# Optimization experiments

Hardware: AMD Instinct MI355X
Metric: run time of the kernel (lower is better)

Reference implementation:

```python
import jax, jax.numpy as jnp
import numpy as np

EMB = 1024
HEADS = 16
HEAD_DIM = EMB // HEADS
B, S = 4, 2048


def setup_inputs() -> dict:
    key = jax.random.key(0)
    ks = jax.random.split(key, 9)
    sc = 1.0 / np.sqrt(EMB)
    x = jax.random.normal(ks[0], (B, S, EMB), dtype=jnp.float32)
    Wq = jax.random.normal(ks[1], (EMB, EMB), dtype=jnp.float32) * sc
    bq = jax.random.normal(ks[2], (EMB,), dtype=jnp.float32) * 0.02
    Wk = jax.random.normal(ks[3], (EMB, EMB), dtype=jnp.float32) * sc
    bk = jax.random.normal(ks[4], (EMB,), dtype=jnp.float32) * 0.02
    Wv = jax.random.normal(ks[5], (EMB, EMB), dtype=jnp.float32) * sc
    bv = jax.random.normal(ks[6], (EMB,), dtype=jnp.float32) * 0.02
    Wo = jax.random.normal(ks[7], (EMB, EMB), dtype=jnp.float32) * sc
    bo = jax.random.normal(ks[8], (EMB,), dtype=jnp.float32) * 0.02
    # causal mask: 1 where allowed (lower triangular), 0 elsewhere
    causal_mask = jnp.tril(jnp.ones((S, S), dtype=jnp.int32))[None, None]
    return {"x": x, "Wq": Wq, "bq": bq, "Wk": Wk, "bk": bk,
            "Wv": Wv, "bv": bv, "Wo": Wo, "bo": bo,
            "causal_mask": causal_mask}


def reference(x, Wq, bq, Wk, bk, Wv, bv, Wo, bo, causal_mask):
    bs, seq, _ = x.shape
    # nn.Linear: x @ W.T + b; then view [bs, seq, H, hd] and transpose to [bs, H, seq, hd]
    def proj(W, b):
        return (x @ W.T + b).reshape(bs, seq, HEADS, HEAD_DIM).transpose(0, 2, 1, 3)
    q, k, v = proj(Wq, bq), proj(Wk, bk), proj(Wv, bv)
    scale = 1.0 / np.sqrt(HEAD_DIM).astype(np.float32)
    dots = jnp.einsum('bhqd,bhkd->bhqk', q, k) * scale  # [B, H, S, S]
    dots = jnp.where(causal_mask == 0, -jnp.inf, dots)
    attn = jax.nn.softmax(dots, axis=-1)
    out = jnp.einsum('bhqk,bhkd->bhqd', attn, v)  # [B, H, S, hd]
    out = out.transpose(0, 2, 1, 3).reshape(bs, seq, EMB)
    return out @ Wo.T + bo
```

## Files before the change

kernel.cpp:

```cpp
#include <hip/hip_runtime.h>
#include <hip/hip_bf16.h>

typedef __attribute__((ext_vector_type(8))) short short8;
typedef __attribute__((ext_vector_type(4))) float floatx4;

#define B_    4
#define S_    2048
#define EMB_  1024
#define NH_   16
#define HD_   64

#if __has_builtin(__builtin_amdgcn_exp2f)
#define EXP2F(x) __builtin_amdgcn_exp2f(x)
#else
#define EXP2F(x) exp2f(x)
#endif

__device__ __forceinline__ void async_cp16(const void* g, void* l) {
  __builtin_amdgcn_global_load_lds(
      (const __attribute__((address_space(1))) unsigned int*)g,
      (__attribute__((address_space(3))) unsigned int*)l, 16, 0, 0);
}

__device__ __forceinline__ ushort4 cvt4(const float4 f) {
  __bf16 t[4] = {(__bf16)f.x, (__bf16)f.y, (__bf16)f.z, (__bf16)f.w};
  return *(const ushort4*)t;
}

__device__ __forceinline__ short8 pack8(const float4 a, const float4 b) {
  union { short8 s; ushort4 u[2]; } r;
  r.u[0] = cvt4(a);
  r.u[1] = cvt4(b);
  return r.s;
}

__global__ __launch_bounds__(256)
void cvt_kernel(const float* __restrict__ x,
                const float* __restrict__ wq, const float* __restrict__ wk,
                const float* __restrict__ wv, const float* __restrict__ wo,
                const float* __restrict__ bq, const float* __restrict__ bk,
                const float* __restrict__ bv,
                __bf16* __restrict__ xb, __bf16* __restrict__ Wcat,
                __bf16* __restrict__ Wob, float* __restrict__ bcat)
{
  const int NX4 = 2097152;
  const int NW4 = 262144;
  int g = blockIdx.x * 256 + threadIdx.x;
  if (g < NX4) {
    *(ushort4*)(xb + (size_t)g * 4) = cvt4(*(const float4*)(x + (size_t)g * 4));
    return;
  }
  g -= NX4;
  if (g < 3 * NW4) {
    const float* src = (g < NW4) ? wq : (g < 2 * NW4) ? wk : wv;
    const int gg = (g < NW4) ? g : (g < 2 * NW4) ? g - NW4 : g - 2 * NW4;
    *(ushort4*)(Wcat + (size_t)g * 4) = cvt4(*(const float4*)(src + (size_t)gg * 4));
    return;
  }
  g -= 3 * NW4;
  if (g < NW4) {
    *(ushort4*)(Wob + (size_t)g * 4) = cvt4(*(const float4*)(wo + (size_t)g * 4));
    return;
  }
  g -= NW4;
  if (g < 768) {
    const float* src = (g < 256) ? bq : (g < 512) ? bk : bv;
    *(float4*)(bcat + (size_t)g * 4) = *(const float4*)(src + (size_t)(g & 255) * 4);
  }
}

__global__ __launch_bounds__(256)
void gemm_qkv_kernel(const __bf16* __restrict__ A, const __bf16* __restrict__ W,
                     const float* __restrict__ bcat,
                     __bf16* __restrict__ Qb, __bf16* __restrict__ Kb,
                     __bf16* __restrict__ Vb)
{
  __shared__ __attribute__((aligned(16))) __bf16 As[128 * 32];
  __shared__ __attribute__((aligned(16))) __bf16 Ws[128 * 32];
  const int tid  = threadIdx.x;
  const int wave = tid >> 6, lane = tid & 63;
  const int l15  = lane & 15, quad = lane >> 4;
  const int wm   = wave >> 1, wn = wave & 1;
  const int bm   = blockIdx.y * 128;
  const int bn   = blockIdx.x * 128;
  const int widx = bn >> 10;
  const float QS = 0.180336880f;

  floatx4 acc[4][4];
#pragma unroll
  for (int i = 0; i < 4; ++i)
#pragma unroll
    for (int j = 0; j < 4; ++j) acc[i][j] = (floatx4){0.f, 0.f, 0.f, 0.f};

  const int srow = tid >> 2;
  const int gcol = (((tid & 3) ^ ((tid >> 3) & 3)) << 3);
  const int xsw  = (l15 >> 1) & 3;
  const __bf16* Ag = A + (size_t)(bm + srow) * 1024 + gcol;
  const __bf16* Wg = W + (size_t)(bn + srow) * 1024 + gcol;
  __bf16* AsD = As + tid * 8;
  __bf16* WsD = Ws + tid * 8;

  for (int k0 = 0; k0 < 1024; k0 += 32) {
    __syncthreads();
    async_cp16(Ag + k0,             AsD);
    async_cp16(Ag + k0 + 64 * 1024, AsD + 2048);
    async_cp16(Wg + k0,             WsD);
    async_cp16(Wg + k0 + 64 * 1024, WsD + 2048);
    __syncthreads();
    short8 af[4], wf[4];
#pragma unroll
    for (int mi = 0; mi < 4; ++mi)
      af[mi] = *(const short8*)(As + ((wm * 64 + mi * 16 + l15) << 5) + ((quad ^ xsw) << 3));
#pragma unroll
    for (int ni = 0; ni < 4; ++ni)
      wf[ni] = *(const short8*)(Ws + ((wn * 64 + ni * 16 + l15) << 5) + ((quad ^ xsw) << 3));
#pragma unroll
    for (int mi = 0; mi < 4; ++mi)
#pragma unroll
      for (int ni = 0; ni < 4; ++ni)
        acc[mi][ni] = __builtin_amdgcn_mfma_f32_16x16x32_bf16(af[mi], wf[ni], acc[mi][ni], 0, 0, 0);
  }

#pragma unroll
  for (int ni = 0; ni < 4; ++ni) {
    const int n  = bn + wn * 64 + ni * 16 + l15;
    const float bvb = bcat[n];
    const int np = n & 1023;
    const int h = np >> 6, d = np & 63;
#pragma unroll
    for (int mi = 0; mi < 4; ++mi) {
      const int m0 = bm + wm * 64 + mi * 16 + quad * 4;
      const int b = m0 >> 11, s0 = m0 & 2047;
      floatx4 v = acc[mi][ni];
      if (widx == 0) {
        const size_t base = (size_t)(b * 16 + h) * (S_ * 64) + d;
#pragma unroll
        for (int r = 0; r < 4; ++r)
          Qb[base + (size_t)(s0 + r) * 64] = (__bf16)((v[r] + bvb) * QS);
      } else if (widx == 1) {
        const size_t base = (size_t)(b * 16 + h) * (S_ * 64) + d;
#pragma unroll
        for (int r = 0; r < 4; ++r)
          Kb[base + (size_t)(s0 + r) * 64] = (__bf16)(v[r] + bvb);
      } else {
        const size_t base = ((size_t)(b * 16 + h) * 64 + d) * S_ + s0;
        union { ushort4 u4; unsigned short u[4]; } pk;
#pragma unroll
        for (int r = 0; r < 4; ++r) {
          __bf16 hv = (__bf16)(v[r] + bvb);
          pk.u[r] = *(unsigned short*)&hv;
        }
        *(ushort4*)(Vb + base) = pk.u4;
      }
    }
  }
}

__device__ __forceinline__ void softmax_update_pf(
    floatx4* s, float& mrun, float& lsum, floatx4* oacc,
    short8& pf0, short8& pf1)
{
  float t0 = fmaxf(fmaxf(s[0][0], s[0][1]), fmaxf(s[0][2], s[0][3]));
  float t1 = fmaxf(fmaxf(s[1][0], s[1][1]), fmaxf(s[1][2], s[1][3]));
  float t2 = fmaxf(fmaxf(s[2][0], s[2][1]), fmaxf(s[2][2], s[2][3]));
  float t3 = fmaxf(fmaxf(s[3][0], s[3][1]), fmaxf(s[3][2], s[3][3]));
  float tmax = fmaxf(fmaxf(t0, t1), fmaxf(t2, t3));
  tmax = fmaxf(tmax, __shfl_xor(tmax, 16));
  tmax = fmaxf(tmax, __shfl_xor(tmax, 32));

  const float mold = mrun;
  if (!__all(tmax <= mold + 8.0f)) {
    const float mnew = fmaxf(mold, tmax);
    const float alpha = EXP2F(mold - mnew);
#pragma unroll
    for (int ni = 0; ni < 4; ++ni)
#pragma unroll
      for (int r = 0; r < 4; ++r) oacc[ni][r] *= alpha;
    lsum *= alpha;
    mrun = mnew;
  }
  const float m = mrun;

  float4 p0, p1, p2, p3;
  p0.x = EXP2F(s[0][0] - m); p0.y = EXP2F(s[0][1] - m);
  p0.z = EXP2F(s[0][2] - m); p0.w = EXP2F(s[0][3] - m);
  p1.x = EXP2F(s[1][0] - m); p1.y = EXP2F(s[1][1] - m);
  p1.z = EXP2F(s[1][2] - m); p1.w = EXP2F(s[1][3] - m);
  p2.x = EXP2F(s[2][0] - m); p2.y = EXP2F(s[2][1] - m);
  p2.z = EXP2F(s[2][2] - m); p2.w = EXP2F(s[2][3] - m);
  p3.x = EXP2F(s[3][0] - m); p3.y = EXP2F(s[3][1] - m);
  p3.z = EXP2F(s[3][2] - m); p3.w = EXP2F(s[3][3] - m);

  lsum += ((p0.x + p0.y) + (p0.z + p0.w)) + ((p1.x + p1.y) + (p1.z + p1.w))
        + ((p2.x + p2.y) + (p2.z + p2.w)) + ((p3.x + p3.y) + (p3.z + p3.w));

  pf0 = pack8(p0, p2);
  pf1 = pack8(p1, p3);
}

__global__ __launch_bounds__(256, 2)
void attn_kernel(__bf16* __restrict__ Q, const __bf16* __restrict__ K,
                 const __bf16* __restrict__ Vt)
{
  __shared__ __attribute__((aligned(16))) __bf16 Ks[64 * 72];
  __shared__ __attribute__((aligned(16))) __bf16 Vs[64 * 72];

  const int tid  = threadIdx.x;
  const int wave = tid >> 6, lane = tid & 63;
  const int l15  = lane & 15, quad = lane >> 4;
  const int qtA  = blockIdx.x, bh = blockIdx.y;
  const size_t hb = (size_t)bh * (S_ * 64);
  const float MASKV = -1.0e30f;

  const int srow = tid >> 3;
  const int scol = (tid & 7) << 3;
  const int prow = ((srow >> 2) & 1) * 32 + ((srow >> 3) & 3) * 4 + (srow & 3);

  for (int qsel = 0; qsel < 2; ++qsel) {
    const int qt = qsel ? (15 - qtA) : qtA;
    const int qw = qt * 128 + wave * 32;
    const int myqA = qw + l15;
    const int myqB = qw + 16 + l15;
    const int nsub = 2 * qt + 2;

    const __bf16* qpA = Q + hb + (size_t)myqA * 64 + quad * 8;
    const __bf16* qpB = Q + hb + (size_t)myqB * 64 + quad * 8;
    short8 aqA0 = *(const short8*)(qpA);
    short8 aqA1 = *(const short8*)(qpA + 32);
    short8 aqB0 = *(const short8*)(qpB);
    short8 aqB1 = *(const short8*)(qpB + 32);

    floatx4 oaccA[4], oaccB[4];
#pragma unroll
    for (int j = 0; j < 4; ++j) {
      oaccA[j] = (floatx4){0.f, 0.f, 0.f, 0.f};
      oaccB[j] = (floatx4){0.f, 0.f, 0.f, 0.f};
    }
    float lsumA = 0.f, lsumB = 0.f;
    float mrunA = MASKV, mrunB = MASKV;

    uint4 kreg0, kreg1, vreg0, vreg1;
    {
      const __bf16* kp = K  + hb + (size_t)srow * 64 + scol;
      const __bf16* vp = Vt + hb + (size_t)srow * S_ + scol;
      kreg0 = *(const uint4*)kp;
      kreg1 = *(const uint4*)(kp + 32 * 64);
      vreg0 = *(const uint4*)vp;
      vreg1 = *(const uint4*)(vp + (size_t)32 * S_);
    }

    for (int kt = 0; kt < nsub; ++kt) {
      __syncthreads();
      *(uint4*)(&Ks[prow * 72 + scol])        = kreg0;
      *(uint4*)(&Ks[(prow + 16) * 72 + scol]) = kreg1;
      *(uint4*)(&Vs[srow * 72 + scol])        = vreg0;
      *(uint4*)(&Vs[(srow + 32) * 72 + scol]) = vreg1;
      __syncthreads();

      if (kt + 1 < nsub) {
        const __bf16* kp = K  + hb + (size_t)((kt + 1) * 64 + srow) * 64 + scol;
        const __bf16* vp = Vt + hb + (size_t)srow * S_ + (kt + 1) * 64 + scol;
        kreg0 = *(const uint4*)kp;
        kreg1 = *(const uint4*)(kp + 32 * 64);
        vreg0 = *(const uint4*)vp;
        vreg1 = *(const uint4*)(vp + (size_t)32 * S_);
      }

      if (kt * 64 <= qw + 31) {
        floatx4 sA[4], sB[4];
#pragma unroll
        for (int j = 0; j < 4; ++j) {
          sA[j] = (floatx4){0.f, 0.f, 0.f, 0.f};
          sB[j] = (floatx4){0.f, 0.f, 0.f, 0.f};
        }
#pragma unroll
        for (int kk = 0; kk < 2; ++kk) {
          const short8 aqa = kk ? aqA1 : aqA0;
          const short8 aqb = kk ? aqB1 : aqB0;
          short8 bk[4];
#pragma unroll
          for (int ni = 0; ni < 4; ++ni)
            bk[ni] = *(const short8*)(&Ks[(ni * 16 + l15) * 72 + kk * 32 + quad * 8]);
#pragma unroll
          for (int ni = 0; ni < 4; ++ni)
            sA[ni] = __builtin_amdgcn_mfma_f32_16x16x32_bf16(bk[ni], aqa, sA[ni], 0, 0, 0);
#pragma unroll
          for (int ni = 0; ni < 4; ++ni)
            sB[ni] = __builtin_amdgcn_mfma_f32_16x16x32_bf16(bk[ni], aqb, sB[ni], 0, 0, 0);
        }

        const int kb2 = kt * 64 + quad * 8;
        if (kt * 64 + 63 > qw) {
#pragma unroll
          for (int ni = 0; ni < 4; ++ni)
#pragma unroll
            for (int r = 0; r < 4; ++r) {
              const int kvg = kb2 + ((ni & 1) << 5) + ((ni >> 1) << 2) + r;
              if (kvg > myqA) sA[ni][r] = MASKV;
            }
        }
        if (kt * 64 + 63 > qw + 16) {
#pragma unroll
          for (int ni = 0; ni < 4; ++ni)
#pragma unroll
            for (int r = 0; r < 4; ++r) {
              const int kvg = kb2 + ((ni & 1) << 5) + ((ni >> 1) << 2) + r;
              if (kvg > myqB) sB[ni][r] = MASKV;
            }
        }

        short8 pfA0, pfA1, pfB0, pfB1;
        softmax_update_pf(sA, mrunA, lsumA, oaccA, pfA0, pfA1);
        softmax_update_pf(sB, mrunB, lsumB, oaccB, pfB0, pfB1);

#pragma unroll
        for (int kk = 0; kk < 2; ++kk) {
          short8 bv[4];
#pragma unroll
          for (int ni = 0; ni < 4; ++ni)
            bv[ni] = *(const short8*)(&Vs[(ni * 16 + l15) * 72 + kk * 32 + quad * 8]);
          const short8 pfA = kk ? pfA1 : pfA0;
          const short8 pfB = kk ? pfB1 : pfB0;
#pragma unroll
          for (int ni = 0; ni < 4; ++ni)
            oaccA[ni] = __builtin_amdgcn_mfma_f32_16x16x32_bf16(bv[ni], pfA, oaccA[ni], 0, 0, 0);
#pragma unroll
          for (int ni = 0; ni < 4; ++ni)
            oaccB[ni] = __builtin_amdgcn_mfma_f32_16x16x32_bf16(bv[ni], pfB, oaccB[ni], 0, 0, 0);
        }
      }
    }

    {
      float l = lsumA;
      l += __shfl_xor(l, 16);
      l += __shfl_xor(l, 32);
      const float inv = 1.0f / fmaxf(l, 1e-20f);
      const size_t rowb = hb + (size_t)myqA * 64;
#pragma unroll
      for (int ni = 0; ni < 4; ++ni) {
        float4 o;
        o.x = oaccA[ni][0] * inv;
        o.y = oaccA[ni][1] * inv;
        o.z = oaccA[ni][2] * inv;
        o.w = oaccA[ni][3] * inv;
        *(ushort4*)(Q + rowb + ni * 16 + quad * 4) = cvt4(o);
      }
    }
    {
      float l = lsumB;
      l += __shfl_xor(l, 16);
      l += __shfl_xor(l, 32);
      const float inv = 1.0f / fmaxf(l, 1e-20f);
      const size_t rowb = hb + (size_t)myqB * 64;
#pragma unroll
      for (int ni = 0; ni < 4; ++ni) {
        float4 o;
        o.x = oaccB[ni][0] * inv;
        o.y = oaccB[ni][1] * inv;
        o.z = oaccB[ni][2] * inv;
        o.w = oaccB[ni][3] * inv;
        *(ushort4*)(Q + rowb + ni * 16 + quad * 4) = cvt4(o);
      }
    }
  }
}

__global__ __launch_bounds__(256)
void gemm_o_kernel(const __bf16* __restrict__ A, const __bf16* __restrict__ W,
                   const float* __restrict__ bias, float* __restrict__ out)
{
  __shared__ __attribute__((aligned(16))) __bf16 As[128 * 32];
  __shared__ __attribute__((aligned(16))) __bf16 Ws[128 * 32];
  const int tid  = threadIdx.x;
  const int wave = tid >> 6, lane = tid & 63;
  const int l15  = lane & 15, quad = lane >> 4;
  const int wm   = wave >> 1, wn = wave & 1;
  const int bm   = blockIdx.y * 128;
  const int bn   = blockIdx.x * 128;

  floatx4 acc[4][4];
#pragma unroll
  for (int i = 0; i < 4; ++i)
#pragma unroll
    for (int j = 0; j < 4; ++j) acc[i][j] = (floatx4){0.f, 0.f, 0.f, 0.f};

  const int srow = tid >> 2;
  const int gcol = (((tid & 3) ^ ((tid >> 3) & 3)) << 3);
  const int xsw  = (l15 >> 1) & 3;
  const __bf16* Wg = W + (size_t)(bn + srow) * 1024 + gcol;
  const int bb = bm >> 11;
  const int ss = (bm & 2047) + srow;
  __bf16* AsD = As + tid * 8;
  __bf16* WsD = Ws + tid * 8;

  for (int k0 = 0; k0 < 1024; k0 += 32) {
    const int c = k0 + gcol, h = c >> 6, dd = c & 63;
    const __bf16* pa0 = A + (((size_t)(bb * 16 + h) * S_) + ss) * 64 + dd;
    __syncthreads();
    async_cp16(pa0,           AsD);
    async_cp16(pa0 + 64 * 64, AsD + 2048);
    async_cp16(Wg + k0,             WsD);
    async_cp16(Wg + k0 + 64 * 1024, WsD + 2048);
    __syncthreads();

    short8 af[4], wf[4];
#pragma unroll
    for (int mi = 0; mi < 4; ++mi)
      af[mi] = *(const short8*)(As + ((wm * 64 + mi * 16 + l15) << 5) + ((quad ^ xsw) << 3));
#pragma unroll
    for (int ni = 0; ni < 4; ++ni)
      wf[ni] = *(const short8*)(Ws + ((wn * 64 + ni * 16 + l15) << 5) + ((quad ^ xsw) << 3));
#pragma unroll
    for (int mi = 0; mi < 4; ++mi)
#pragma unroll
      for (int ni = 0; ni < 4; ++ni)
        acc[mi][ni] = __builtin_amdgcn_mfma_f32_16x16x32_bf16(af[mi], wf[ni], acc[mi][ni], 0, 0, 0);
  }

#pragma unroll
  for (int ni = 0; ni < 4; ++ni) {
    const int n = bn + wn * 64 + ni * 16 + l15;
    const float bvb = bias[n];
#pragma unroll
    for (int mi = 0; mi < 4; ++mi) {
      const int m0 = bm + wm * 64 + mi * 16 + quad * 4;
      floatx4 v = acc[mi][ni];
#pragma unroll
      for (int r = 0; r < 4; ++r)
        out[(size_t)(m0 + r) * 1024 + n] = v[r] + bvb;
    }
  }
}

extern "C" void kernel_launch(void* const* d_in, const int* in_sizes, int n_in,
                              void* d_out, int out_size, void* d_ws, size_t ws_size,
                              hipStream_t stream) {
  const float* x  = (const float*)d_in[0];
  const float* Wq = (const float*)d_in[1];
  const float* bq = (const float*)d_in[2];
  const float* Wk = (const float*)d_in[3];
  const float* bk = (const float*)d_in[4];
  const float* Wv = (const float*)d_in[5];
  const float* bv = (const float*)d_in[6];
  const float* Wo = (const float*)d_in[7];
  const float* bo = (const float*)d_in[8];

  const size_t BUF = (size_t)B_ * NH_ * S_ * HD_;
  __bf16* ws   = (__bf16*)d_ws;
  __bf16* xb   = ws;
  __bf16* Wcat = ws + 8388608;
  __bf16* Wob  = ws + 11534336;
  __bf16* Qb   = ws + 12582912;
  float*  bcat = (float*)(ws + 20971520);
  __bf16* Kb   = (__bf16*)d_out;
  __bf16* Vb   = (__bf16*)d_out + BUF;

  dim3 blk(256);
  cvt_kernel<<<12291, blk, 0, stream>>>(x, Wq, Wk, Wv, Wo, bq, bk, bv,
                                        xb, Wcat, Wob, bcat);
  gemm_qkv_kernel<<<dim3(24, 64), blk, 0, stream>>>(xb, Wcat, bcat, Qb, Kb, Vb);
  attn_kernel<<<dim3(8, 64), blk, 0, stream>>>(Qb, Kb, Vb);
  gemm_o_kernel<<<dim3(8, 64), blk, 0, stream>>>(Qb, Wob, bo, (float*)d_out);
}
```

Measured before the change: 276.3 us.

## Fuse x fp32-to-bf16 conversion into QKV GEMM loads, raise MFMA wave priority

The separate pass that converted x to bf16 in the workspace is removed. The QKV GEMM now loads fp32 x directly into registers, prefetched one k-step ahead, and packs it to bf16 before storing to LDS. This drops a full 32 MB read and 16 MB write and shrinks the conversion launch. The cost is that each x tile is read as fp32 and converted once for each of the 24 N-blocks, replacing the async global-to-LDS copy with register loads. The attention kernel also wraps its MFMA groups in s_setprio to favour matrix-issuing waves.

```diff
diff --git a/kernel.cpp b/kernel.cpp
--- a/kernel.cpp
+++ b/kernel.cpp
@@ -35,22 +35,15 @@
 }
 
 __global__ __launch_bounds__(256)
-void cvt_kernel(const float* __restrict__ x,
-                const float* __restrict__ wq, const float* __restrict__ wk,
+void cvt_kernel(const float* __restrict__ wq, const float* __restrict__ wk,
                 const float* __restrict__ wv, const float* __restrict__ wo,
                 const float* __restrict__ bq, const float* __restrict__ bk,
                 const float* __restrict__ bv,
-                __bf16* __restrict__ xb, __bf16* __restrict__ Wcat,
-                __bf16* __restrict__ Wob, float* __restrict__ bcat)
+                __bf16* __restrict__ Wcat, __bf16* __restrict__ Wob,
+                float* __restrict__ bcat)
 {
-  const int NX4 = 2097152;
   const int NW4 = 262144;
   int g = blockIdx.x * 256 + threadIdx.x;
-  if (g < NX4) {
-    *(ushort4*)(xb + (size_t)g * 4) = cvt4(*(const float4*)(x + (size_t)g * 4));
-    return;
-  }
-  g -= NX4;
   if (g < 3 * NW4) {
     const float* src = (g < NW4) ? wq : (g < 2 * NW4) ? wk : wv;
     const int gg = (g < NW4) ? g : (g < 2 * NW4) ? g - NW4 : g - 2 * NW4;
@@ -70,7 +63,7 @@
 }
 
 __global__ __launch_bounds__(256)
-void gemm_qkv_kernel(const __bf16* __restrict__ A, const __bf16* __restrict__ W,
+void gemm_qkv_kernel(const float* __restrict__ X, const __bf16* __restrict__ W,
                      const float* __restrict__ bcat,
                      __bf16* __restrict__ Qb, __bf16* __restrict__ Kb,
                      __bf16* __restrict__ Vb)
@@ -95,18 +88,30 @@
   const int srow = tid >> 2;
   const int gcol = (((tid & 3) ^ ((tid >> 3) & 3)) << 3);
   const int xsw  = (l15 >> 1) & 3;
-  const __bf16* Ag = A + (size_t)(bm + srow) * 1024 + gcol;
+  const float*  Ag = X + (size_t)(bm + srow) * 1024 + gcol;
   const __bf16* Wg = W + (size_t)(bn + srow) * 1024 + gcol;
   __bf16* AsD = As + tid * 8;
   __bf16* WsD = Ws + tid * 8;
 
+  float4 a00, a01, a10, a11;
+  a00 = *(const float4*)(Ag);
+  a01 = *(const float4*)(Ag + 4);
+  a10 = *(const float4*)(Ag + 64 * 1024);
+  a11 = *(const float4*)(Ag + 64 * 1024 + 4);
+
   for (int k0 = 0; k0 < 1024; k0 += 32) {
     __syncthreads();
-    async_cp16(Ag + k0,             AsD);
-    async_cp16(Ag + k0 + 64 * 1024, AsD + 2048);
+    *(short8*)(AsD)        = pack8(a00, a01);
+    *(short8*)(AsD + 2048) = pack8(a10, a11);
     async_cp16(Wg + k0,             WsD);
     async_cp16(Wg + k0 + 64 * 1024, WsD + 2048);
     __syncthreads();
+    if (k0 + 32 < 1024) {
+      a00 = *(const float4*)(Ag + k0 + 32);
+      a01 = *(const float4*)(Ag + k0 + 36);
+      a10 = *(const float4*)(Ag + k0 + 32 + 64 * 1024);
+      a11 = *(const float4*)(Ag + k0 + 36 + 64 * 1024);
+    }
     short8 af[4], wf[4];
 #pragma unroll
     for (int mi = 0; mi < 4; ++mi)
@@ -281,12 +286,14 @@
 #pragma unroll
           for (int ni = 0; ni < 4; ++ni)
             bk[ni] = *(const short8*)(&Ks[(ni * 16 + l15) * 72 + kk * 32 + quad * 8]);
+          __builtin_amdgcn_s_setprio(1);
 #pragma unroll
           for (int ni = 0; ni < 4; ++ni)
             sA[ni] = __builtin_amdgcn_mfma_f32_16x16x32_bf16(bk[ni], aqa, sA[ni], 0, 0, 0);
 #pragma unroll
           for (int ni = 0; ni < 4; ++ni)
             sB[ni] = __builtin_amdgcn_mfma_f32_16x16x32_bf16(bk[ni], aqb, sB[ni], 0, 0, 0);
+          __builtin_amdgcn_s_setprio(0);
         }
 
         const int kb2 = kt * 64 + quad * 8;
@@ -321,12 +328,14 @@
             bv[ni] = *(const short8*)(&Vs[(ni * 16 + l15) * 72 + kk * 32 + quad * 8]);
           const short8 pfA = kk ? pfA1 : pfA0;
           const short8 pfB = kk ? pfB1 : pfB0;
+          __builtin_amdgcn_s_setprio(1);
 #pragma unroll
           for (int ni = 0; ni < 4; ++ni)
             oaccA[ni] = __builtin_amdgcn_mfma_f32_16x16x32_bf16(bv[ni], pfA, oaccA[ni], 0, 0, 0);
 #pragma unroll
           for (int ni = 0; ni < 4; ++ni)
             oaccB[ni] = __builtin_amdgcn_mfma_f32_16x16x32_bf16(bv[ni], pfB, oaccB[ni], 0, 0, 0);
+          __builtin_amdgcn_s_setprio(0);
         }
       }
     }
@@ -448,18 +457,17 @@
 
   const size_t BUF = (size_t)B_ * NH_ * S_ * HD_;
   __bf16* ws   = (__bf16*)d_ws;
-  __bf16* xb   = ws;
-  __bf16* Wcat = ws + 8388608;
-  __bf16* Wob  = ws + 11534336;
-  __bf16* Qb   = ws + 12582912;
-  float*  bcat = (float*)(ws + 20971520);
+  __bf16* Wcat = ws;
+  __bf16* Wob  = ws + 3145728;
+  __bf16* Qb   = ws + 4194304;
+  float*  bcat = (float*)(ws + 12582912);
   __bf16* Kb   = (__bf16*)d_out;
   __bf16* Vb   = (__bf16*)d_out + BUF;
 
   dim3 blk(256);
-  cvt_kernel<<<12291, blk, 0, stream>>>(x, Wq, Wk, Wv, Wo, bq, bk, bv,
-                                        xb, Wcat, Wob, bcat);
-  gemm_qkv_kernel<<<dim3(24, 64), blk, 0, stream>>>(xb, Wcat, bcat, Qb, Kb, Vb);
+  cvt_kernel<<<4099, blk, 0, stream>>>(Wq, Wk, Wv, Wo, bq, bk, bv,
+                                       Wcat, Wob, bcat);
+  gemm_qkv_kernel<<<dim3(24, 64), blk, 0, stream>>>(x, Wcat, bcat, Qb, Kb, Vb);
   attn_kernel<<<dim3(8, 64), blk, 0, stream>>>(Qb, Kb, Vb);
   gemm_o_kernel<<<dim3(8, 64), blk, 0, stream>>>(Qb, Wob, bo, (float*)d_out);
 }
```

Measured after the change: 289.8 us. 1.05x slower.
